# Optimization experiments

Measured on AMD Instinct MI355X. Metric: run time of the kernel, lower is better.

The kernel has to match this reference:

```python
import jax, jax.numpy as jnp
import numpy as np
import math

H, KV, D, HID, WIN = 8, 4, 256, 2048, 1024  # heads, kv heads, head_dim, hidden, sliding window
B, S = 1, 2048

def _rms(x, scale):
    # Gemma3RMSNorm: hardcoded 1e-6 eps, (1+scale) gain
    var = jnp.mean(jnp.square(x), axis=-1, keepdims=True)
    return x * jax.lax.rsqrt(var + 1e-6) * (1.0 + scale)

def _rot_half(x):
    x1, x2 = jnp.split(x, 2, axis=-1)
    return jnp.concatenate((-x2, x1), axis=-1)

def setup_inputs() -> dict:
    key = jax.random.key(0)
    ks = jax.random.split(key, 8)
    x = jax.random.normal(ks[0], (B, S, HID), jnp.float32)
    attn_mask = jnp.ones((B, S), jnp.bool_)
    segment_pos = jnp.broadcast_to(jnp.arange(S, dtype=jnp.int32)[None], (B, S))
    # true RoPE tables, theta=1e6 (Gemma3 global layers)
    inv_freq = 1.0 / (1e6 ** (np.arange(0, D, 2, dtype=np.float32) / D))
    ang = np.arange(S, dtype=np.float32)[:, None] * inv_freq[None, :]  # [S, D/2]
    emb = np.concatenate([ang, ang], axis=-1)                          # [S, D]
    cos = jnp.asarray(np.cos(emb), jnp.float32)[None]                  # [1, S, D]
    sin = jnp.asarray(np.sin(emb), jnp.float32)[None]
    sd = 1.0 / math.sqrt(HID)
    wq = jax.random.normal(ks[1], (HID, H * D), jnp.float32) * sd
    wk = jax.random.normal(ks[2], (HID, KV * D), jnp.float32) * sd
    wv = jax.random.normal(ks[3], (HID, KV * D), jnp.float32) * sd
    wo = jax.random.normal(ks[4], (H * D, HID), jnp.float32) * (1.0 / math.sqrt(H * D))
    q_scale = jnp.zeros((D,), jnp.float32)  # zeros_init as in module
    k_scale = jnp.zeros((D,), jnp.float32)
    return dict(x=x, attn_mask=attn_mask, segment_pos=segment_pos, cos=cos, sin=sin,
                wq=wq, wk=wk, wv=wv, wo=wo, q_scale=q_scale, k_scale=k_scale)

def reference(x, attn_mask, segment_pos, cos, sin, wq, wk, wv, wo, q_scale, k_scale):
    b, s, _ = x.shape
    # projections -> [b, h, s, d]
    q = (x @ wq).reshape(b, s, H, D).transpose(0, 2, 1, 3)
    k = (x @ wk).reshape(b, s, KV, D).transpose(0, 2, 1, 3)
    v = (x @ wv).reshape(b, s, KV, D).transpose(0, 2, 1, 3)
    # per-head QK RMSNorm
    q = _rms(q, q_scale)
    k = _rms(k, k_scale)
    # RoPE (cos/sin broadcast over head axis, unsqueeze_dim=1)
    c, sn = cos[:, None], sin[:, None]
    q = q * c + _rot_half(q) * sn
    k = k * c + _rot_half(k) * sn
    # GQA: repeat-interleave kv heads
    rep = H // KV
    k = jnp.repeat(k, rep, axis=1)
    v = jnp.repeat(v, rep, axis=1)
    scores = jnp.einsum('bhqd,bhkd->bhqk', q, k) / math.sqrt(D)
    # causal + padding mask (q_len > 1 path, no image bidirectional mask)
    causal = jnp.tril(jnp.ones((s, s), jnp.bool_))
    mask = causal[None] & attn_mask[:, None, :]          # [b, q, kv]
    # sliding window mask (prefill: cache positions = arange)
    kvpos = jnp.arange(s)
    pos = segment_pos[:, :, None]
    sliding = (kvpos[None, None] > pos - WIN) & (kvpos[None, None] < pos + WIN)
    full = mask & sliding
    scores = scores + jnp.where(full[:, None], 0.0, -1e37)
    w = jax.nn.softmax(scores.astype(jnp.float32), axis=-1).astype(scores.dtype)
    out = jnp.einsum('bhqk,bhkd->bhqd', w, v)
    out = out.transpose(0, 2, 1, 3).reshape(b, s, H * D)
    return out @ wo
```

## Files before the change

kernel.cpp:

```cpp
#include <hip/hip_runtime.h>
#include <hip/hip_bf16.h>

#define S_LEN 2048
#define HID 2048
#define NH 8
#define NKV 4
#define HD 256
#define WIN 1024

typedef __hip_bfloat16 bf16;
typedef __attribute__((ext_vector_type(8))) short bf16x8;
typedef __attribute__((ext_vector_type(4))) float f32x4;

__device__ __forceinline__ void gld_lds16(void* lds, const void* g) {
    __builtin_amdgcn_global_load_lds(
        (const __attribute__((address_space(1))) unsigned int*)g,
        (__attribute__((address_space(3))) unsigned int*)lds,
        16, 0, 0);
}


__device__ __forceinline__ void transT_body(const float* __restrict__ src, bf16* __restrict__ dst,
                                            int R, int C, int r0, int c0) {
    __shared__ bf16 Ts[64][72];
    const int tid = threadIdx.x;
    {
        const int r = tid >> 2;
        const int cq = (tid & 3) * 16;
#pragma unroll
        for (int j = 0; j < 16; j += 4) {
            float4 v = *(const float4*)&src[(size_t)(r0 + r) * C + c0 + cq + j];
            Ts[cq + j + 0][r] = __float2bfloat16(v.x);
            Ts[cq + j + 1][r] = __float2bfloat16(v.y);
            Ts[cq + j + 2][r] = __float2bfloat16(v.z);
            Ts[cq + j + 3][r] = __float2bfloat16(v.w);
        }
    }
    __syncthreads();
    {
        const int c = tid >> 2;
        const int rq = (tid & 3) * 16;
#pragma unroll
        for (int j = 0; j < 16; j += 8)
            *(uint4*)&dst[(size_t)(c0 + c) * R + r0 + rq + j] = *(const uint4*)&Ts[c][rq + j];
    }
}

__global__ __launch_bounds__(256)
void prep_all(const float* __restrict__ xf, const float* __restrict__ wqf,
              const float* __restrict__ wkf, const float* __restrict__ wvf,
              const float* __restrict__ wof,
              bf16* __restrict__ xb, bf16* __restrict__ wqkvt, bf16* __restrict__ wot) {
    const int bid = blockIdx.x;
    if (bid < 2048) {
        const int i = bid * 256 + threadIdx.x;
        float4 a = ((const float4*)xf)[i * 2];
        float4 b = ((const float4*)xf)[i * 2 + 1];
        union { uint4 v; bf16 h[8]; } u;
        u.h[0] = __float2bfloat16(a.x); u.h[1] = __float2bfloat16(a.y);
        u.h[2] = __float2bfloat16(a.z); u.h[3] = __float2bfloat16(a.w);
        u.h[4] = __float2bfloat16(b.x); u.h[5] = __float2bfloat16(b.y);
        u.h[6] = __float2bfloat16(b.z); u.h[7] = __float2bfloat16(b.w);
        ((uint4*)xb)[i] = u.v;
    } else if (bid < 4096) {
        const int t = bid - 2048;
        const int bx = t & 63, by = t >> 6;
        const float* src; int C, c0, drow0;
        if (bx < 32)      { src = wqf; C = 2048; c0 = bx * 64;        drow0 = bx * 64; }
        else if (bx < 48) { src = wkf; C = 1024; c0 = (bx - 32) * 64; drow0 = 2048 + (bx - 32) * 64; }
        else              { src = wvf; C = 1024; c0 = (bx - 48) * 64; drow0 = 3072 + (bx - 48) * 64; }
        bf16* dshift = wqkvt + ((size_t)drow0 - c0) * HID;
        transT_body(src, dshift, HID, C, by * 64, c0);
    } else {
        const int t = bid - 4096;
        const int bx = t & 31, by = t >> 5;
        transT_body(wof, wot, NH * HD, HID, by * 64, bx * 64);
    }
}

template<int MODE>
__global__ __launch_bounds__(512, 2)
void gemm8p(const bf16* __restrict__ A, const bf16* __restrict__ Bt,
            bf16* __restrict__ Cb,
            bf16* __restrict__ Qo, bf16* __restrict__ Ko, bf16* __restrict__ Vto) {
    extern __shared__ bf16 smem[];
    bf16* AsP = smem;
    bf16* BsP = smem + 3 * 256 * 64;

    const int tid = threadIdx.x;
    const int w = tid >> 6, lane = tid & 63;
    const int lnm = lane & 15, quad = lane >> 4;
    const int wr = w >> 1, wc = w & 1;
    const int r8 = lane >> 3;
    const int swz = ((lane & 7) ^ r8) * 8;

    const int bid = blockIdx.x;
    const int xcd = bid & 7, idx = bid >> 3;
    int m0, n0, kbeg, nt;
    size_t zoff = 0;
    if constexpr (MODE == 1) {
        const int m_t = (xcd >> 2) * 4 + (idx >> 3);
        const int n_t = (xcd & 3) * 8 + (idx & 7);
        m0 = m_t * 256; n0 = n_t * 128; kbeg = 0; nt = 2048 / 64;
    } else {
        const int z   = xcd >> 2;
        const int n_t = (xcd & 3) * 4 + (idx & 3);
        const int m_t = idx >> 2;
        m0 = m_t * 256; n0 = n_t * 128; kbeg = z * 1024; nt = 1024 / 64;
        zoff = (size_t)z * 2048 * 2048;
    }
    const int K = 2048;

    const bf16* pA[4];
#pragma unroll
    for (int g = 0; g < 4; ++g)
        pA[g] = A + (size_t)(m0 + w * 32 + g * 8 + r8) * K + kbeg + swz;
    const bf16* pB[2];
#pragma unroll
    for (int g = 0; g < 2; ++g)
        pB[g] = Bt + (size_t)(n0 + w * 16 + g * 8 + r8) * K + kbeg + swz;
    const int dA = w * 32 * 64;
    const int dB = w * 16 * 64;

#define STG_A(slot, g, t) gld_lds16(AsP + (slot) * 16384 + dA + (g) * 512, pA[g] + (t) * 64)
#define STG_B(slot, g, t) gld_lds16(BsP + (slot) * 8192  + dB + (g) * 512, pB[g] + (t) * 64)
#define LDFRAG(base, row, kh) \
    (*(const bf16x8*)((base) + (row) * 64 + (((((kh) << 2) | quad) ^ ((row) & 7)) << 3)))

    f32x4 acc[4][4];
#pragma unroll
    for (int i = 0; i < 4; ++i)
#pragma unroll
        for (int j = 0; j < 4; ++j) acc[i][j] = (f32x4){0.f, 0.f, 0.f, 0.f};

    STG_A(0, 0, 0); STG_A(0, 1, 0); STG_A(0, 2, 0); STG_A(0, 3, 0);
    STG_B(0, 0, 0); STG_B(0, 1, 0);
    STG_A(1, 0, 1); STG_A(1, 1, 1); STG_A(1, 2, 1); STG_A(1, 3, 1);
    STG_B(1, 0, 1); STG_B(1, 1, 1);
    asm volatile("s_waitcnt vmcnt(6)" ::: "memory");
    __builtin_amdgcn_sched_barrier(0);
    __builtin_amdgcn_s_barrier();

    int sc = 0;
    for (int t = 0; t < nt; ++t) {
        const int ss = (sc == 0) ? 2 : sc - 1;
        const bf16* As_ = AsP + sc * 16384;
        const bf16* Bs_ = BsP + sc * 8192;
        const bool pf = (t + 2 < nt);

        bf16x8 a0[2][2], b[4][2];
#pragma unroll
        for (int tm = 0; tm < 2; ++tm)
#pragma unroll
            for (int kh = 0; kh < 2; ++kh)
                a0[tm][kh] = LDFRAG(As_, wr * 64 + tm * 16 + lnm, kh);
#pragma unroll
        for (int tn = 0; tn < 4; ++tn)
#pragma unroll
            for (int kh = 0; kh < 2; ++kh)
                b[tn][kh] = LDFRAG(Bs_, wc * 64 + tn * 16 + lnm, kh);
        if (pf) { STG_A(ss, 0, t + 2); STG_A(ss, 1, t + 2); STG_B(ss, 0, t + 2); }
        __builtin_amdgcn_s_barrier();
        asm volatile("s_waitcnt lgkmcnt(0)" ::: "memory");
        __builtin_amdgcn_sched_barrier(0);
        __builtin_amdgcn_s_setprio(1);
#pragma unroll
        for (int kh = 0; kh < 2; ++kh)
#pragma unroll
            for (int tm = 0; tm < 2; ++tm)
#pragma unroll
                for (int tn = 0; tn < 4; ++tn)
                    acc[tm][tn] = __builtin_amdgcn_mfma_f32_16x16x32_bf16(
                        a0[tm][kh], b[tn][kh], acc[tm][tn], 0, 0, 0);
        __builtin_amdgcn_s_setprio(0);
        __builtin_amdgcn_s_barrier();

        bf16x8 a1[2][2];
#pragma unroll
        for (int tm = 0; tm < 2; ++tm)
#pragma unroll
            for (int kh = 0; kh < 2; ++kh)
                a1[tm][kh] = LDFRAG(As_, wr * 64 + (tm + 2) * 16 + lnm, kh);
        if (pf) { STG_A(ss, 2, t + 2); STG_A(ss, 3, t + 2); STG_B(ss, 1, t + 2); }
        if (pf) { asm volatile("s_waitcnt vmcnt(6)" ::: "memory"); }
        else    { asm volatile("s_waitcnt vmcnt(0)" ::: "memory"); }
        __builtin_amdgcn_sched_barrier(0);
        __builtin_amdgcn_s_barrier();
        asm volatile("s_waitcnt lgkmcnt(0)" ::: "memory");
        __builtin_amdgcn_sched_barrier(0);
        __builtin_amdgcn_s_setprio(1);
#pragma unroll
        for (int kh = 0; kh < 2; ++kh)
#pragma unroll
            for (int tm = 0; tm < 2; ++tm)
#pragma unroll
                for (int tn = 0; tn < 4; ++tn)
                    acc[tm + 2][tn] = __builtin_amdgcn_mfma_f32_16x16x32_bf16(
                        a1[tm][kh], b[tn][kh], acc[tm + 2][tn], 0, 0, 0);
        __builtin_amdgcn_s_setprio(0);
        __builtin_amdgcn_s_barrier();

        sc = (sc == 2) ? 0 : sc + 1;
    }
#undef STG_A
#undef STG_B
#undef LDFRAG

#pragma unroll
    for (int tm = 0; tm < 4; ++tm)
#pragma unroll
        for (int tn = 0; tn < 4; ++tn)
#pragma unroll
            for (int r = 0; r < 4; ++r) {
                const int row = m0 + wr * 64 + tm * 16 + quad * 4 + r;
                const int col = n0 + wc * 64 + tn * 16 + lnm;
                const float v = acc[tm][tn][r];
                if constexpr (MODE == 2) {
                    Cb[zoff + (size_t)row * 2048 + col] = __float2bfloat16(v);
                } else {
                    if (col < 2048)
                        Qo[(size_t)row * (NH * HD) + col] = __float2bfloat16(v);
                    else if (col < 3072)
                        Ko[(size_t)row * (NKV * HD) + col - 2048] = __float2bfloat16(v);
                    else
                        Vto[(size_t)(col - 3072) * S_LEN + row] = __float2bfloat16(v);
                }
            }
}

__global__ __launch_bounds__(256)
void splitk_add(const bf16* __restrict__ p, float* __restrict__ out) {
    const int i = blockIdx.x * 256 + threadIdx.x;
    union { uint4 v; bf16 h[8]; } a, b;
    a.v = ((const uint4*)p)[i];
    b.v = ((const uint4*)(p + (size_t)2048 * 2048))[i];
    float4 o0, o1;
    o0.x = (float)a.h[0] + (float)b.h[0]; o0.y = (float)a.h[1] + (float)b.h[1];
    o0.z = (float)a.h[2] + (float)b.h[2]; o0.w = (float)a.h[3] + (float)b.h[3];
    o1.x = (float)a.h[4] + (float)b.h[4]; o1.y = (float)a.h[5] + (float)b.h[5];
    o1.z = (float)a.h[6] + (float)b.h[6]; o1.w = (float)a.h[7] + (float)b.h[7];
    ((float4*)out)[i * 2]     = o0;
    ((float4*)out)[i * 2 + 1] = o1;
}

__global__ __launch_bounds__(256)
void rmsrope_kernel(bf16* __restrict__ Q, bf16* __restrict__ Kb,
                    const float* __restrict__ cosb, const float* __restrict__ sinb,
                    const float* __restrict__ qscale, const float* __restrict__ kscale,
                    float qmul) {
    __shared__ float cf[256], sf[256], qsl[256], ksl[256];
    const int p = blockIdx.x;
    const int tid = threadIdx.x, w = tid >> 6, lane = tid & 63;

    cf[tid]  = cosb[(size_t)p * HD + tid];
    sf[tid]  = sinb[(size_t)p * HD + tid];
    qsl[tid] = qscale[tid];
    ksl[tid] = kscale[tid];
    __syncthreads();

    const int d0 = lane * 2;
    const float c0 = cf[d0],       c1 = cf[d0 + 1];
    const float cA = cf[d0 + 128], cB = cf[d0 + 129];
    const float s0 = sf[d0],       s1 = sf[d0 + 1];
    const float sA = sf[d0 + 128], sB = sf[d0 + 129];

#pragma unroll
    for (int i = 0; i < 3; ++i) {
        const int hg = w + i * 4;
        bf16* base;
        const float* scl;
        float mul;
        if (hg < NH) { base = Q + (size_t)p * (NH * HD) + hg * HD; scl = qsl; mul = qmul; }
        else         { base = Kb + (size_t)p * (NKV * HD) + (hg - NH) * HD; scl = ksl; mul = 1.f; }

        float x0 = (float)base[d0],       x1 = (float)base[d0 + 1];
        float y0 = (float)base[d0 + 128], y1 = (float)base[d0 + 129];

        float ss = x0 * x0 + x1 * x1 + y0 * y0 + y1 * y1;
#pragma unroll
        for (int off = 32; off > 0; off >>= 1) ss += __shfl_xor(ss, off, 64);
        const float r = rsqrtf(ss * (1.0f / (float)HD) + 1e-6f);

        x0 *= r * (1.f + scl[d0]);
        x1 *= r * (1.f + scl[d0 + 1]);
        y0 *= r * (1.f + scl[d0 + 128]);
        y1 *= r * (1.f + scl[d0 + 129]);

        base[d0]       = __float2bfloat16((x0 * c0 - y0 * s0) * mul);
        base[d0 + 1]   = __float2bfloat16((x1 * c1 - y1 * s1) * mul);
        base[d0 + 128] = __float2bfloat16((y0 * cA + x0 * sA) * mul);
        base[d0 + 129] = __float2bfloat16((y1 * cB + x1 * sB) * mul);
    }
}

#define NCHUNK 4

__device__ __forceinline__ unsigned pkbf(float a, float b) {
    union { bf16 h; unsigned short u; } ca, cb;
    ca.h = __float2bfloat16(a); cb.h = __float2bfloat16(b);
    return (unsigned)ca.u | ((unsigned)cb.u << 16);
}

__global__ __launch_bounds__(512)
void attn_mfma(const bf16* __restrict__ Q, const bf16* __restrict__ K,
               const bf16* __restrict__ Vt, bf16* __restrict__ Op,
               float2* __restrict__ ml) {
    __shared__ bf16 Ks[2][32][256];
    __shared__ bf16 Vs[256][32];
    const int qt = blockIdx.x, h = blockIdx.y, chunk = blockIdx.z, kvh = h >> 1;
    const int tid = threadIdx.x, w = tid >> 6, lane = tid & 63;
    const int lnm = lane & 15, quad = lane >> 4;

    bf16x8 qf[8];
    const int qrow = qt * 128 + w * 16 + lnm;
#pragma unroll
    for (int s = 0; s < 8; ++s)
        qf[s] = *(const bf16x8*)&Q[(size_t)qrow * HID + h * HD + s * 32 + quad * 8];

    f32x4 o[16];
#pragma unroll
    for (int i = 0; i < 16; ++i) o[i] = (f32x4){0.f, 0.f, 0.f, 0.f};
    float M = -3e38f, L = 0.f;

    const int ktlo = (qt >= 8) ? (4 * qt - 32) : 0;
    const int kthi = 4 * qt + 3;
    const int ntile = kthi - ktlo + 1;
    const int c0 = ktlo + (chunk * ntile) / NCHUNK;
    const int c1 = ktlo + ((chunk + 1) * ntile) / NCHUNK - 1;

    const int srow = w * 4 + (lane >> 5);
    const int sunit = lane & 31;
    const bf16* kg = K + (size_t)kvh * HD;
    const int vrow = lane >> 2;
    const int vgu  = (lane & 3) ^ ((lane >> 3) & 3);
    const bf16* vsrc = Vt + ((size_t)(kvh * HD + w * 32 + vrow)) * S_LEN + vgu * 8;

#define STAGE_K(kt_, buf_)                                                        \
    {                                                                             \
        _Pragma("unroll")                                                         \
        for (int cc = 0; cc < 2; ++cc) {                                          \
            const int r_ = srow + cc * 2;                                         \
            const int ug_ = sunit ^ (r_ & 7);                                     \
            gld_lds16(&Ks[buf_][w * 4 + cc * 2][0],                               \
                      kg + (size_t)((kt_) * 32 + r_) * (NKV * HD) + ug_ * 8);     \
        }                                                                         \
    }
#define STAGE_V(kt_)                                                              \
    {                                                                             \
        _Pragma("unroll")                                                         \
        for (int cc = 0; cc < 2; ++cc)                                            \
            gld_lds16(&Vs[w * 32 + cc * 16][0],                                   \
                      vsrc + (size_t)cc * 16 * S_LEN + (kt_) * 32);               \
    }
#define KFRAG(buf_, t_, s_) \
    (*(const bf16x8*)&Ks[buf_][(t_) * 16 + lnm][((((s_) * 4 + quad) ^ (lnm & 7)) * 8)])
#define VFRAG(t2_) \
    (*(const bf16x8*)&Vs[(t2_) * 16 + lnm][(quad ^ ((lnm >> 1) & 3)) * 8])

    if (c0 <= c1) {
        STAGE_K(c0, 0);
        asm volatile("s_waitcnt vmcnt(0)" ::: "memory");
        __builtin_amdgcn_sched_barrier(0);
        __builtin_amdgcn_s_barrier();

        for (int kt = c0; kt <= c1; ++kt) {
            const int buf = (kt - c0) & 1;
            STAGE_V(kt);
            if (kt < c1) STAGE_K(kt + 1, buf ^ 1);

            f32x4 s4[2];
            s4[0] = (f32x4){0.f, 0.f, 0.f, 0.f};
            s4[1] = (f32x4){0.f, 0.f, 0.f, 0.f};
            __builtin_amdgcn_s_setprio(1);
#pragma unroll
            for (int t = 0; t < 2; ++t)
#pragma unroll
                for (int s = 0; s < 8; ++s)
                    s4[t] = __builtin_amdgcn_mfma_f32_16x16x32_bf16(
                        KFRAG(buf, t, s), qf[s], s4[t], 0, 0, 0);
            __builtin_amdgcn_s_setprio(0);

#pragma unroll
            for (int t = 0; t < 2; ++t)
#pragma unroll
                for (int r = 0; r < 4; ++r) {
                    const int n_g = kt * 32 + t * 16 + quad * 4 + r;
                    if (n_g > qrow || n_g + (WIN - 1) < qrow) s4[t][r] = -1e30f;
                }

            float mx = fmaxf(fmaxf(fmaxf(s4[0][0], s4[0][1]), fmaxf(s4[0][2], s4[0][3])),
                             fmaxf(fmaxf(s4[1][0], s4[1][1]), fmaxf(s4[1][2], s4[1][3])));
            mx = fmaxf(mx, __shfl_xor(mx, 16, 64));
            mx = fmaxf(mx, __shfl_xor(mx, 32, 64));

            if (!__all(mx <= M + 8.f)) {
                const float Mn = fmaxf(M, mx);
                const float al = __expf(M - Mn);
                M = Mn;
                L *= al;
                float alr[4];
#pragma unroll
                for (int r = 0; r < 4; ++r) alr[r] = __shfl(al, quad * 4 + r, 64);
#pragma unroll
                for (int t2 = 0; t2 < 16; ++t2)
#pragma unroll
                    for (int r = 0; r < 4; ++r) o[t2][r] *= alr[r];
            }

            float rs = 0.f;
            unsigned u00, u01, u10, u11;
            {
                float p0 = __expf(s4[0][0] - M), p1 = __expf(s4[0][1] - M);
                float p2 = __expf(s4[0][2] - M), p3 = __expf(s4[0][3] - M);
                rs += (p0 + p1) + (p2 + p3);
                u00 = pkbf(p0, p1); u01 = pkbf(p2, p3);
                p0 = __expf(s4[1][0] - M); p1 = __expf(s4[1][1] - M);
                p2 = __expf(s4[1][2] - M); p3 = __expf(s4[1][3] - M);
                rs += (p0 + p1) + (p2 + p3);
                u10 = pkbf(p0, p1); u11 = pkbf(p2, p3);
            }
            rs += __shfl_xor(rs, 16, 64);
            rs += __shfl_xor(rs, 32, 64);
            L += rs;

            const int slo = lnm + 16 * (2 * (quad & 1));
            const int shi = slo + 16;
            const int A0 = __shfl((int)u00, slo, 64), A1 = __shfl((int)u01, slo, 64);
            const int A2 = __shfl((int)u00, shi, 64), A3 = __shfl((int)u01, shi, 64);
            const int B0 = __shfl((int)u10, slo, 64), B1 = __shfl((int)u11, slo, 64);
            const int B2 = __shfl((int)u10, shi, 64), B3 = __shfl((int)u11, shi, 64);
            union { bf16x8 v; int i4[4]; } pa;
            pa.i4[0] = (quad < 2) ? A0 : B0;
            pa.i4[1] = (quad < 2) ? A1 : B1;
            pa.i4[2] = (quad < 2) ? A2 : B2;
            pa.i4[3] = (quad < 2) ? A3 : B3;

            if (kt < c1) { asm volatile("s_waitcnt vmcnt(2)" ::: "memory"); }
            else         { asm volatile("s_waitcnt vmcnt(0)" ::: "memory"); }
            __builtin_amdgcn_sched_barrier(0);
            __builtin_amdgcn_s_barrier();

            __builtin_amdgcn_s_setprio(1);
#pragma unroll
            for (int t2 = 0; t2 < 16; ++t2)
                o[t2] = __builtin_amdgcn_mfma_f32_16x16x32_bf16(pa.v, VFRAG(t2), o[t2], 0, 0, 0);
            __builtin_amdgcn_s_setprio(0);

            if (kt < c1) {
                asm volatile("s_waitcnt vmcnt(0) lgkmcnt(0)" ::: "memory");
                __builtin_amdgcn_sched_barrier(0);
                __builtin_amdgcn_s_barrier();
            }
        }
    }
#undef STAGE_K
#undef STAGE_V
#undef KFRAG
#undef VFRAG

    const float rL = (L > 0.f) ? (1.f / L) : 0.f;
    float rr[4];
#pragma unroll
    for (int r = 0; r < 4; ++r) rr[r] = __shfl(rL, quad * 4 + r, 64);
    bf16* Opc = Op + (size_t)chunk * S_LEN * HID;
#pragma unroll
    for (int t2 = 0; t2 < 16; ++t2)
#pragma unroll
        for (int r = 0; r < 4; ++r)
            Opc[(size_t)(qt * 128 + w * 16 + quad * 4 + r) * HID + h * HD + t2 * 16 + lnm] =
                __float2bfloat16(o[t2][r] * rr[r]);
    if (quad == 0)
        ml[((size_t)chunk * S_LEN + qt * 128 + w * 16 + lnm) * NH + h] = make_float2(M, L);
}

__global__ __launch_bounds__(256)
void attn_combine(const bf16* __restrict__ Op, const float2* __restrict__ ml,
                  bf16* __restrict__ O) {
    const int row = blockIdx.x, t = threadIdx.x;
    const int h = t >> 5;
    float2 c[NCHUNK];
    float Mx = -3e38f;
#pragma unroll
    for (int i = 0; i < NCHUNK; ++i) {
        c[i] = ml[((size_t)i * S_LEN + row) * NH + h];
        Mx = fmaxf(Mx, c[i].x);
    }
    float wsum = 0.f, wgt[NCHUNK];
#pragma unroll
    for (int i = 0; i < NCHUNK; ++i) {
        wgt[i] = c[i].y * __expf(c[i].x - Mx);
        wsum += wgt[i];
    }
    const float inv = 1.0f / wsum;
    const size_t base = (size_t)row * HID + t * 8;
    float acc[8] = {0.f, 0.f, 0.f, 0.f, 0.f, 0.f, 0.f, 0.f};
#pragma unroll
    for (int i = 0; i < NCHUNK; ++i) {
        union { uint4 v; bf16 h8[8]; } a;
        a.v = *(const uint4*)(Op + (size_t)i * S_LEN * HID + base);
#pragma unroll
        for (int j = 0; j < 8; ++j) acc[j] += wgt[i] * (float)a.h8[j];
    }
    union { uint4 v; bf16 h8[8]; } ou;
#pragma unroll
    for (int j = 0; j < 8; ++j) ou.h8[j] = __float2bfloat16(acc[j] * inv);
    *(uint4*)(O + base) = ou.v;
}

extern "C" void kernel_launch(void* const* d_in, const int* in_sizes, int n_in,
                              void* d_out, int out_size, void* d_ws, size_t ws_size,
                              hipStream_t stream) {
    const float* xf   = (const float*)d_in[0];
    const float* cosb = (const float*)d_in[3];
    const float* sinb = (const float*)d_in[4];
    const float* wqf  = (const float*)d_in[5];
    const float* wkf  = (const float*)d_in[6];
    const float* wvf  = (const float*)d_in[7];
    const float* wof  = (const float*)d_in[8];
    const float* qs   = (const float*)d_in[9];
    const float* ks   = (const float*)d_in[10];
    float* out = (float*)d_out;
    char* ws = (char*)d_ws;

    bf16*   wot   = (bf16*)(ws);
    bf16*   Qb    = (bf16*)(ws + ( 8ull << 20));
    bf16*   Kb    = (bf16*)(ws + (16ull << 20));
    bf16*   Vtb   = (bf16*)(ws + (20ull << 20));
    bf16*   wqkvt = (bf16*)(ws + (24ull << 20));
    bf16*   xb    = (bf16*)(ws + (40ull << 20));
    bf16*   Op    = (bf16*)(ws + (24ull << 20));
    bf16*   Ab    = (bf16*)(ws + (40ull << 20));
    bf16*   pk    = (bf16*)(ws + (24ull << 20));
    float2* ml    = (float2*)(ws + (56ull << 20));

    dim3 blk(256);

    static bool attr_done = false;
    if (!attr_done) {
        (void)hipFuncSetAttribute(reinterpret_cast<const void*>(gemm8p<1>),
                                  hipFuncAttributeMaxDynamicSharedMemorySize, 147456);
        (void)hipFuncSetAttribute(reinterpret_cast<const void*>(gemm8p<2>),
                                  hipFuncAttributeMaxDynamicSharedMemorySize, 147456);
        attr_done = true;
    }

    prep_all<<<5120, blk, 0, stream>>>(xf, wqf, wkf, wvf, wof, xb, wqkvt, wot);

    gemm8p<1><<<dim3(256), dim3(512), 147456, stream>>>(
        xb, wqkvt, nullptr, Qb, Kb, Vtb);

    rmsrope_kernel<<<dim3(S_LEN), blk, 0, stream>>>(
        Qb, Kb, cosb, sinb, qs, ks, 0.0625f);

    attn_mfma<<<dim3(S_LEN / 128, NH, NCHUNK), dim3(512), 0, stream>>>(
        Qb, Kb, Vtb, Op, ml);
    attn_combine<<<dim3(S_LEN), blk, 0, stream>>>(Op, ml, Ab);

    gemm8p<2><<<dim3(256), dim3(512), 147456, stream>>>(
        Ab, wot, pk, nullptr, nullptr, nullptr);
    splitk_add<<<2048, blk, 0, stream>>>(pk, out);
}
```

Measured before the change: 259.7 us.

## Double-buffer V tiles in attention and fuse split-K reduction via atomics

The attention kernel moves its K and V tiles to dynamic shared memory and double-buffers V alongside K. The per-iteration trailing barrier becomes a single wait-and-barrier at the top of each iteration, so loads of the next tile overlap compute. The output GEMM's split-K partials are now added with float atomics straight into a zeroed output buffer, which removes the bf16 partial round-trip and the separate splitk_add kernel. The cost is an extra memset plus atomic contention, and the sum order of the two halves is no longer deterministic.

```diff
diff --git a/kernel.cpp b/kernel.cpp
--- a/kernel.cpp
+++ b/kernel.cpp
@@ -81,7 +81,7 @@
 template<int MODE>
 __global__ __launch_bounds__(512, 2)
 void gemm8p(const bf16* __restrict__ A, const bf16* __restrict__ Bt,
-            bf16* __restrict__ Cb,
+            float* __restrict__ Outf,
             bf16* __restrict__ Qo, bf16* __restrict__ Ko, bf16* __restrict__ Vto) {
     extern __shared__ bf16 smem[];
     bf16* AsP = smem;
@@ -97,7 +97,6 @@
     const int bid = blockIdx.x;
     const int xcd = bid & 7, idx = bid >> 3;
     int m0, n0, kbeg, nt;
-    size_t zoff = 0;
     if constexpr (MODE == 1) {
         const int m_t = (xcd >> 2) * 4 + (idx >> 3);
         const int n_t = (xcd & 3) * 8 + (idx & 7);
@@ -107,7 +106,6 @@
         const int n_t = (xcd & 3) * 4 + (idx & 3);
         const int m_t = idx >> 2;
         m0 = m_t * 256; n0 = n_t * 128; kbeg = z * 1024; nt = 1024 / 64;
-        zoff = (size_t)z * 2048 * 2048;
     }
     const int K = 2048;
 
@@ -216,7 +214,7 @@
                 const int col = n0 + wc * 64 + tn * 16 + lnm;
                 const float v = acc[tm][tn][r];
                 if constexpr (MODE == 2) {
-                    Cb[zoff + (size_t)row * 2048 + col] = __float2bfloat16(v);
+                    atomicAdd(&Outf[(size_t)row * 2048 + col], v);
                 } else {
                     if (col < 2048)
                         Qo[(size_t)row * (NH * HD) + col] = __float2bfloat16(v);
@@ -229,21 +227,6 @@
 }
 
 __global__ __launch_bounds__(256)
-void splitk_add(const bf16* __restrict__ p, float* __restrict__ out) {
-    const int i = blockIdx.x * 256 + threadIdx.x;
-    union { uint4 v; bf16 h[8]; } a, b;
-    a.v = ((const uint4*)p)[i];
-    b.v = ((const uint4*)(p + (size_t)2048 * 2048))[i];
-    float4 o0, o1;
-    o0.x = (float)a.h[0] + (float)b.h[0]; o0.y = (float)a.h[1] + (float)b.h[1];
-    o0.z = (float)a.h[2] + (float)b.h[2]; o0.w = (float)a.h[3] + (float)b.h[3];
-    o1.x = (float)a.h[4] + (float)b.h[4]; o1.y = (float)a.h[5] + (float)b.h[5];
-    o1.z = (float)a.h[6] + (float)b.h[6]; o1.w = (float)a.h[7] + (float)b.h[7];
-    ((float4*)out)[i * 2]     = o0;
-    ((float4*)out)[i * 2 + 1] = o1;
-}
-
-__global__ __launch_bounds__(256)
 void rmsrope_kernel(bf16* __restrict__ Q, bf16* __restrict__ Kb,
                     const float* __restrict__ cosb, const float* __restrict__ sinb,
                     const float* __restrict__ qscale, const float* __restrict__ kscale,
@@ -305,8 +288,9 @@
 void attn_mfma(const bf16* __restrict__ Q, const bf16* __restrict__ K,
                const bf16* __restrict__ Vt, bf16* __restrict__ Op,
                float2* __restrict__ ml) {
-    __shared__ bf16 Ks[2][32][256];
-    __shared__ bf16 Vs[256][32];
+    extern __shared__ bf16 smem[];
+    bf16* KsP = smem;
+    bf16* VsP = smem + 2 * 32 * 256;
     const int qt = blockIdx.x, h = blockIdx.y, chunk = blockIdx.z, kvh = h >> 1;
     const int tid = threadIdx.x, w = tid >> 6, lane = tid & 63;
     const int lnm = lane & 15, quad = lane >> 4;
@@ -341,32 +325,33 @@
         for (int cc = 0; cc < 2; ++cc) {                                          \
             const int r_ = srow + cc * 2;                                         \
             const int ug_ = sunit ^ (r_ & 7);                                     \
-            gld_lds16(&Ks[buf_][w * 4 + cc * 2][0],                               \
+            gld_lds16(KsP + (buf_) * 8192 + (w * 4 + cc * 2) * 256,               \
                       kg + (size_t)((kt_) * 32 + r_) * (NKV * HD) + ug_ * 8);     \
         }                                                                         \
     }
-#define STAGE_V(kt_)                                                              \
+#define STAGE_V(kt_, vb_)                                                         \
     {                                                                             \
         _Pragma("unroll")                                                         \
         for (int cc = 0; cc < 2; ++cc)                                            \
-            gld_lds16(&Vs[w * 32 + cc * 16][0],                                   \
+            gld_lds16(VsP + (vb_) * 8192 + (w * 32 + cc * 16) * 32,               \
                       vsrc + (size_t)cc * 16 * S_LEN + (kt_) * 32);               \
     }
 #define KFRAG(buf_, t_, s_) \
-    (*(const bf16x8*)&Ks[buf_][(t_) * 16 + lnm][((((s_) * 4 + quad) ^ (lnm & 7)) * 8)])
-#define VFRAG(t2_) \
-    (*(const bf16x8*)&Vs[(t2_) * 16 + lnm][(quad ^ ((lnm >> 1) & 3)) * 8])
+    (*(const bf16x8*)&KsP[(buf_) * 8192 + ((t_) * 16 + lnm) * 256 + ((((s_) * 4 + quad) ^ (lnm & 7)) * 8)])
+#define VFRAG(vb_, t2_) \
+    (*(const bf16x8*)&VsP[(vb_) * 8192 + ((t2_) * 16 + lnm) * 32 + ((quad ^ ((lnm >> 1) & 3)) * 8)])
 
     if (c0 <= c1) {
         STAGE_K(c0, 0);
-        asm volatile("s_waitcnt vmcnt(0)" ::: "memory");
-        __builtin_amdgcn_sched_barrier(0);
-        __builtin_amdgcn_s_barrier();
 
         for (int kt = c0; kt <= c1; ++kt) {
             const int buf = (kt - c0) & 1;
-            STAGE_V(kt);
+            STAGE_V(kt, buf);
             if (kt < c1) STAGE_K(kt + 1, buf ^ 1);
+            if (kt < c1) { asm volatile("s_waitcnt vmcnt(4)" ::: "memory"); }
+            else         { asm volatile("s_waitcnt vmcnt(2)" ::: "memory"); }
+            __builtin_amdgcn_sched_barrier(0);
+            __builtin_amdgcn_s_barrier();
 
             f32x4 s4[2];
             s4[0] = (f32x4){0.f, 0.f, 0.f, 0.f};
@@ -443,14 +428,8 @@
             __builtin_amdgcn_s_setprio(1);
 #pragma unroll
             for (int t2 = 0; t2 < 16; ++t2)
-                o[t2] = __builtin_amdgcn_mfma_f32_16x16x32_bf16(pa.v, VFRAG(t2), o[t2], 0, 0, 0);
+                o[t2] = __builtin_amdgcn_mfma_f32_16x16x32_bf16(pa.v, VFRAG(buf, t2), o[t2], 0, 0, 0);
             __builtin_amdgcn_s_setprio(0);
-
-            if (kt < c1) {
-                asm volatile("s_waitcnt vmcnt(0) lgkmcnt(0)" ::: "memory");
-                __builtin_amdgcn_sched_barrier(0);
-                __builtin_amdgcn_s_barrier();
-            }
         }
     }
 #undef STAGE_K
@@ -530,7 +509,6 @@
     bf16*   xb    = (bf16*)(ws + (40ull << 20));
     bf16*   Op    = (bf16*)(ws + (24ull << 20));
     bf16*   Ab    = (bf16*)(ws + (40ull << 20));
-    bf16*   pk    = (bf16*)(ws + (24ull << 20));
     float2* ml    = (float2*)(ws + (56ull << 20));
 
     dim3 blk(256);
@@ -541,8 +519,12 @@
                                   hipFuncAttributeMaxDynamicSharedMemorySize, 147456);
         (void)hipFuncSetAttribute(reinterpret_cast<const void*>(gemm8p<2>),
                                   hipFuncAttributeMaxDynamicSharedMemorySize, 147456);
+        (void)hipFuncSetAttribute(reinterpret_cast<const void*>(attn_mfma),
+                                  hipFuncAttributeMaxDynamicSharedMemorySize, 65536);
         attr_done = true;
     }
+
+    hipMemsetAsync(out, 0, out_size, stream);
 
     prep_all<<<5120, blk, 0, stream>>>(xf, wqf, wkf, wvf, wof, xb, wqkvt, wot);
 
@@ -552,11 +534,10 @@
     rmsrope_kernel<<<dim3(S_LEN), blk, 0, stream>>>(
         Qb, Kb, cosb, sinb, qs, ks, 0.0625f);
 
-    attn_mfma<<<dim3(S_LEN / 128, NH, NCHUNK), dim3(512), 0, stream>>>(
+    attn_mfma<<<dim3(S_LEN / 128, NH, NCHUNK), dim3(512), 65536, stream>>>(
         Qb, Kb, Vtb, Op, ml);
     attn_combine<<<dim3(S_LEN), blk, 0, stream>>>(Op, ml, Ab);
 
     gemm8p<2><<<dim3(256), dim3(512), 147456, stream>>>(
-        Ab, wot, pk, nullptr, nullptr, nullptr);
-    splitk_add<<<2048, blk, 0, stream>>>(pk, out);
-}
+        Ab, wot, out, nullptr, nullptr, nullptr);
+}
```

New measurement: 273.6 us. 1.05x slower.
